# Optimization experiments

Hardware: AMD Instinct MI355X
Metric: run time of the kernel (lower is better)

Reference implementation:

```python
import jax, jax.numpy as jnp
import numpy as np

D_MODEL = 1024
N_HEADS = 16
HEAD_DIM = D_MODEL // N_HEADS
N_MEM = 16
EPS = 1e-5
ROPE_THETA = 10000.0


def layernorm(x, g, b):
    mu = jnp.mean(x, axis=-1, keepdims=True)
    var = jnp.mean(jnp.square(x - mu), axis=-1, keepdims=True)
    return (x - mu) * jax.lax.rsqrt(var + EPS) * g + b


def rope_cos_sin(seq_len, head_dim, dtype):
    inv_freq = 1.0 / (ROPE_THETA ** (jnp.arange(0, head_dim, 2, dtype=jnp.float32) / head_dim))
    pos = jnp.arange(seq_len, dtype=jnp.float32)
    freqs = pos[:, None] * inv_freq[None, :]            # [S, hd/2]
    emb = jnp.concatenate([freqs, freqs], axis=-1)       # [S, hd]
    return jnp.cos(emb).astype(dtype), jnp.sin(emb).astype(dtype)


def rotate_half(x):
    x1, x2 = jnp.split(x, 2, axis=-1)
    return jnp.concatenate([-x2, x1], axis=-1)


def setup_inputs() -> dict:
    key = jax.random.key(0)
    ks = jax.random.split(key, 8)
    B, T, D = 2, 2048, D_MODEL
    x = jax.random.normal(ks[0], (B, T, D), dtype=jnp.float32)
    memory_tokens = jax.random.normal(ks[1], (1, N_MEM, D), dtype=jnp.float32) * 0.02
    s = 1.0 / np.sqrt(D)
    qkv_w = jax.random.uniform(ks[2], (3 * D, D), minval=-s, maxval=s, dtype=jnp.float32)
    qkv_b = jax.random.uniform(ks[3], (3 * D,), minval=-s, maxval=s, dtype=jnp.float32)
    out_w = jax.random.uniform(ks[4], (D, D), minval=-s, maxval=s, dtype=jnp.float32)
    out_b = jax.random.uniform(ks[5], (D,), minval=-s, maxval=s, dtype=jnp.float32)
    norm_g = jnp.ones((D,), jnp.float32)
    norm_b = jnp.zeros((D,), jnp.float32)
    normm_g = jnp.ones((D,), jnp.float32)
    normm_b = jnp.zeros((D,), jnp.float32)
    return {"x": x, "memory_tokens": memory_tokens, "qkv_w": qkv_w, "qkv_b": qkv_b,
            "out_w": out_w, "out_b": out_b, "norm_g": norm_g, "norm_b": norm_b,
            "normm_g": normm_g, "normm_b": normm_b}


def reference(x, memory_tokens, qkv_w, qkv_b, out_w, out_b, norm_g, norm_b, normm_g, normm_b):
    B, T, D = x.shape
    S = N_MEM + T
    residual = x
    x_norm = layernorm(x, norm_g, norm_b)
    mem = layernorm(jnp.broadcast_to(memory_tokens, (B, N_MEM, D)), normm_g, normm_b)
    xm = jnp.concatenate([mem, x_norm], axis=1)                # [B, S, D]
    qkv = xm @ qkv_w.T + qkv_b                                 # [B, S, 3D]
    qkv = qkv.reshape(B, S, 3, N_HEADS, HEAD_DIM)
    q = jnp.transpose(qkv[:, :, 0], (0, 2, 1, 3))              # [B, H, S, hd]
    k = jnp.transpose(qkv[:, :, 1], (0, 2, 1, 3))
    v = jnp.transpose(qkv[:, :, 2], (0, 2, 1, 3))
    cos, sin = rope_cos_sin(S, HEAD_DIM, x.dtype)              # [S, hd]
    q = q * cos + rotate_half(q) * sin
    k = k * cos + rotate_half(k) * sin
    scale = 1.0 / np.sqrt(HEAD_DIM)
    scores = jnp.einsum("bhqd,bhkd->bhqk", q, k) * scale       # [B, H, S, S]
    causal = jnp.tril(jnp.ones((S, S), dtype=bool))
    scores = jnp.where(causal, scores, jnp.finfo(scores.dtype).min)
    attn = jax.nn.softmax(scores, axis=-1)
    out = jnp.einsum("bhqk,bhkd->bhqd", attn, v)               # [B, H, S, hd]
    out = jnp.transpose(out, (0, 2, 1, 3)).reshape(B, S, D)
    out = out @ out_w.T + out_b
    out = out[:, N_MEM:, :]
    return residual + out
```

## Files before the change

### kernel.cpp

```cpp
#include <hip/hip_runtime.h>
#include <cstdint>


using bf16 = __bf16;
typedef __attribute__((ext_vector_type(8))) __bf16 bf16x8;
typedef __attribute__((ext_vector_type(4))) __bf16 bf16x4;
typedef __attribute__((ext_vector_type(4))) float floatx4;

#define MFMA16(a, b, c) __builtin_amdgcn_mfma_f32_16x16x32_bf16(a, b, c, 0, 0, 0)

constexpr int SV = 2064;
constexpr int SP = 2112;
constexpr float LOG2_THETA = 13.287712379549449f;

__device__ __forceinline__ bool dt_is_bf16(const void* p) {
  return *(const uint32_t*)p == 0x3F803F80u;
}

struct f8 { float v[8]; };

__device__ __forceinline__ f8 load8(const void* p, size_t idx, bool bf) {
  f8 r;
  if (bf) {
    bf16x8 t = *(const bf16x8*)((const bf16*)p + idx);
#pragma unroll
    for (int j = 0; j < 8; ++j) r.v[j] = (float)t[j];
  } else {
    float4 a = *(const float4*)((const float*)p + idx);
    float4 b = *(const float4*)((const float*)p + idx + 4);
    r.v[0] = a.x; r.v[1] = a.y; r.v[2] = a.z; r.v[3] = a.w;
    r.v[4] = b.x; r.v[5] = b.y; r.v[6] = b.z; r.v[7] = b.w;
  }
  return r;
}

__device__ __forceinline__ float ld1(const void* p, size_t idx, bool bf) {
  return bf ? (float)((const bf16*)p)[idx] : ((const float*)p)[idx];
}

__device__ __forceinline__ void load16_to_lds(const bf16* gptr, bf16* lptr) {
  auto* g = reinterpret_cast<const __attribute__((address_space(1))) uint32_t*>(
      reinterpret_cast<uintptr_t>(gptr));
  auto* l = reinterpret_cast<__attribute__((address_space(3))) uint32_t*>(
      reinterpret_cast<uintptr_t>(lptr));
  __builtin_amdgcn_global_load_lds(g, l, 16, 0, 0);
}

__device__ __forceinline__ unsigned cvtpk_bf16(float lo, float hi) {
  unsigned r;
  asm("v_cvt_pk_bf16_f32 %0, %1, %2" : "=v"(r) : "v"(lo), "v"(hi));
  return r;
}

__global__ __launch_bounds__(256) void conv_w(
    const void* __restrict__ W, const void* __restrict__ flagp,
    bf16* __restrict__ dst) {
  const bool bf = dt_is_bf16(flagp);
  const size_t i = ((size_t)blockIdx.x * 256 + threadIdx.x) * 8;
  const f8 v = load8(W, i, bf);
  bf16x8 o;
#pragma unroll
  for (int j = 0; j < 8; ++j) o[j] = (bf16)v.v[j];
  *(bf16x8*)&dst[i] = o;
}

__global__ __launch_bounds__(256) void rope_tab(float2* __restrict__ tab) {
  const int i = blockIdx.x * 256 + threadIdx.x;
  const int pos = i >> 5, f = i & 31;
  const float ang = (float)pos * exp2f((float)f * (-LOG2_THETA / 32.0f));
  float c, s;
  sincosf(ang, &c, &s);
  tab[i] = make_float2(c, s);
}

__global__ __launch_bounds__(256) void ln_all(
    const void* __restrict__ x, const void* __restrict__ mem,
    const void* __restrict__ ng, const void* __restrict__ nb,
    const void* __restrict__ mg, const void* __restrict__ mb,
    bf16* __restrict__ mem16, bf16* __restrict__ xln) {
  const bool bf = dt_is_bf16(ng);
  const int t = threadIdx.x, wid = t >> 6, lane = t & 63;
  const int row = blockIdx.x * 4 + wid;
  const void *src, *g, *bb;
  size_t soff;
  bf16* out;
  if (row < 16) {
    src = mem; soff = (size_t)row * 1024; g = mg; bb = mb;
    out = mem16 + (size_t)row * 1024;
  } else {
    src = x; soff = (size_t)(row - 16) * 1024; g = ng; bb = nb;
    out = xln + (size_t)(row - 16) * 1024;
  }
  const f8 v0 = load8(src, soff + lane * 8, bf);
  const f8 v1 = load8(src, soff + 512 + lane * 8, bf);
  float sum = 0.f, sq = 0.f;
#pragma unroll
  for (int j = 0; j < 8; ++j) { sum += v0.v[j]; sq += v0.v[j] * v0.v[j]; }
#pragma unroll
  for (int j = 0; j < 8; ++j) { sum += v1.v[j]; sq += v1.v[j] * v1.v[j]; }
#pragma unroll
  for (int off = 1; off < 64; off <<= 1) {
    sum += __shfl_xor(sum, off);
    sq += __shfl_xor(sq, off);
  }
  const float mu = sum * (1.0f / 1024.0f);
  const float var = sq * (1.0f / 1024.0f) - mu * mu;
  const float rstd = rsqrtf(var + 1e-5f);
  const f8 g0 = load8(g, lane * 8, bf), g1 = load8(g, 512 + lane * 8, bf);
  const f8 b0 = load8(bb, lane * 8, bf), b1 = load8(bb, 512 + lane * 8, bf);
  bf16x8 o0, o1;
#pragma unroll
  for (int j = 0; j < 8; ++j) {
    o0[j] = (bf16)((v0.v[j] - mu) * rstd * g0.v[j] + b0.v[j]);
    o1[j] = (bf16)((v1.v[j] - mu) * rstd * g1.v[j] + b1.v[j]);
  }
  *(bf16x8*)&out[lane * 8] = o0;
  *(bf16x8*)&out[512 + lane * 8] = o1;
}

__global__ __launch_bounds__(512, 1) void gemm0_rope(
    const bf16* __restrict__ mem16, const bf16* __restrict__ xln,
    const bf16* __restrict__ Wqb, const void* __restrict__ bias,
    const void* __restrict__ flagp, const float2* __restrict__ rtab,
    bf16* __restrict__ Qg, bf16* __restrict__ Kg, bf16* __restrict__ Vg) {
  const bool bf = dt_is_bf16(flagp);
  __shared__ bf16 SH[65536];
  const int t = threadIdx.x;
  const int row0 = blockIdx.x * 256;
  const int col0 = blockIdx.y * 256;
  const int wid = t >> 6, lane = t & 63, lr = lane & 15, lg = lane >> 4;
  const int wm = wid >> 2, wn = wid & 3;
  const int xorv = (lr & 7) << 3;

  const int coff = (((t & 7) ^ ((t >> 3) & 7)) << 3);
  const bf16* aptr[4];
  const bf16* bptr[4];
#pragma unroll
  for (int s = 0; s < 4; ++s) {
    int g = row0 + s * 64 + (t >> 3);
    if (g > 4127) g = 4127;
    const int b2 = (g >= SV) ? 1 : 0;
    const int ss = g - b2 * SV;
    const bf16* ap = (ss < 16) ? (mem16 + (size_t)ss * 1024)
                               : (xln + ((size_t)(b2 * 2048 + ss - 16)) * 1024);
    aptr[s] = ap + coff;
    bptr[s] = Wqb + (size_t)(col0 + s * 64 + (t >> 3)) * 1024 + coff;
  }

  const int ldsbase = (t & ~63) * 8;
  auto STAGE = [&](int bufi, int k0) {
    bf16* Ld = SH + bufi * 32768;
#pragma unroll
    for (int s = 0; s < 4; ++s)
      load16_to_lds(aptr[s] + k0, Ld + s * 4096 + ldsbase);
#pragma unroll
    for (int s = 0; s < 4; ++s)
      load16_to_lds(bptr[s] + k0, Ld + 16384 + s * 4096 + ldsbase);
  };

  floatx4 acc[8][4] = {};
  STAGE(0, 0);
  STAGE(1, 64);

  for (int kt = 0; kt < 16; ++kt) {
    const int cur = kt & 1;
    if (kt < 15)
      asm volatile("s_waitcnt vmcnt(8)" ::: "memory");
    else
      asm volatile("s_waitcnt vmcnt(0)" ::: "memory");
    __builtin_amdgcn_s_barrier();
    __builtin_amdgcn_sched_barrier(0);
    const bf16* Ab = SH + cur * 32768;
    const bf16* Bb = Ab + 16384;
    bf16x8 a0[8], b0[4], a1[8], b1[4];
#pragma unroll
    for (int mi = 0; mi < 8; ++mi)
      a0[mi] = *(const bf16x8*)&Ab[(wm * 128 + mi * 16 + lr) * 64 + ((lg * 8) ^ xorv)];
#pragma unroll
    for (int ni = 0; ni < 4; ++ni)
      b0[ni] = *(const bf16x8*)&Bb[(wn * 64 + ni * 16 + lr) * 64 + ((lg * 8) ^ xorv)];
    __builtin_amdgcn_s_setprio(1);
#pragma unroll
    for (int mi = 0; mi < 8; ++mi)
#pragma unroll
      for (int ni = 0; ni < 4; ++ni)
        acc[mi][ni] = MFMA16(a0[mi], b0[ni], acc[mi][ni]);
    __builtin_amdgcn_s_setprio(0);
#pragma unroll
    for (int mi = 0; mi < 8; ++mi)
      a1[mi] = *(const bf16x8*)&Ab[(wm * 128 + mi * 16 + lr) * 64 + ((32 + lg * 8) ^ xorv)];
#pragma unroll
    for (int ni = 0; ni < 4; ++ni)
      b1[ni] = *(const bf16x8*)&Bb[(wn * 64 + ni * 16 + lr) * 64 + ((32 + lg * 8) ^ xorv)];
    __builtin_amdgcn_sched_barrier(0);
    asm volatile("s_waitcnt lgkmcnt(0)" ::: "memory");
    __builtin_amdgcn_s_barrier();
    __builtin_amdgcn_sched_barrier(0);
    if (kt < 14) STAGE(cur, (kt + 2) * 64);
    __builtin_amdgcn_s_setprio(1);
#pragma unroll
    for (int mi = 0; mi < 8; ++mi)
#pragma unroll
      for (int ni = 0; ni < 4; ++ni)
        acc[mi][ni] = MFMA16(a1[mi], b1[ni], acc[mi][ni]);
    __builtin_amdgcn_s_setprio(0);
  }

  const int colbase = col0 + wn * 64;
  const int part = colbase >> 10;
  const int h = (colbase >> 6) & 15;
  const int row0w = row0 + wm * 128;

  if (part == 2) {
#pragma unroll
    for (int mi = 0; mi < 8; ++mi) {
      const int gq = row0w + mi * 16 + lg * 4;
      if (gq >= 2 * SV) continue;
      const int b2 = (gq >= SV) ? 1 : 0;
      const int pos = gq - b2 * SV;
      const size_t hb = (size_t)(b2 * 16 + h) * 64;
#pragma unroll
      for (int ni = 0; ni < 4; ++ni) {
        const int d = ni * 16 + lr;
        const float bc = ld1(bias, colbase + ni * 16 + lr, bf);
        bf16x4 vv;
#pragma unroll
        for (int r = 0; r < 4; ++r) vv[r] = (bf16)(acc[mi][ni][r] + bc);
        *(bf16x4*)&Vg[(hb + d) * SP + pos] = vv;
      }
    }
  } else {
    bf16* Dst = (part == 0) ? Qg : Kg;
    const float qs = (part == 0) ? 0.18033688011f : 1.0f;
    float bv[4];
#pragma unroll
    for (int a = 0; a < 4; ++a) bv[a] = ld1(bias, colbase + a * 16 + lr, bf);
#pragma unroll
    for (int mi = 0; mi < 8; ++mi) {
#pragma unroll
      for (int r = 0; r < 4; ++r) {
        const int g = row0w + mi * 16 + lg * 4 + r;
        if (g >= 2 * SV) continue;
        const int b2 = (g >= SV) ? 1 : 0;
        const int pos = g - b2 * SV;
        bf16* drow = Dst + ((size_t)(b2 * 16 + h) * SP + pos) * 64;
#pragma unroll
        for (int a = 0; a < 2; ++a) {
          const float2 cs = rtab[pos * 32 + a * 16 + lr];
          const float vlo = (acc[mi][a][r] + bv[a]) * qs;
          const float vhi = (acc[mi][a + 2][r] + bv[a + 2]) * qs;
          drow[a * 16 + lr] = (bf16)(vlo * cs.x - vhi * cs.y);
          drow[32 + a * 16 + lr] = (bf16)(vhi * cs.x + vlo * cs.y);
        }
      }
    }
  }
}

__device__ __forceinline__ void softmax_pack(const floatx4* c, int qrow, int k0,
                                             bool nm, int lg, float& lsum,
                                             unsigned (&paw)[2][4]) {
  float pr[4][4];
#pragma unroll
  for (int j2 = 0; j2 < 4; ++j2) {
#pragma unroll
    for (int rr = 0; rr < 4; ++rr) {
      float s = c[j2][rr];
      if (nm && (k0 + j2 * 16 + lg * 4 + rr > qrow)) s = -1e30f;
      float p;
      asm("v_exp_f32 %0, %1" : "=v"(p) : "v"(s));
      lsum += p;
      pr[j2][rr] = p;
    }
  }
#pragma unroll
  for (int cc = 0; cc < 2; ++cc) {
#pragma unroll
    for (int p_ = 0; p_ < 2; ++p_) {
      unsigned a = cvtpk_bf16(pr[2 * cc][2 * p_], pr[2 * cc][2 * p_ + 1]);
      unsigned b2 = cvtpk_bf16(pr[2 * cc + 1][2 * p_], pr[2 * cc + 1][2 * p_ + 1]);
      asm("v_permlane32_swap_b32 %0, %1" : "+v"(a), "+v"(b2));
      asm("v_permlane16_swap_b32 %0, %1" : "+v"(a), "+v"(b2));
      paw[cc][p_] = a;
      paw[cc][2 + p_] = b2;
    }
  }
}

__global__ __launch_bounds__(256) void flash3(
    const bf16* __restrict__ Qg, const bf16* __restrict__ Kg,
    const bf16* __restrict__ Vg, bf16* __restrict__ attn_out) {
  const int st = 16 - blockIdx.x;
  const int bh = blockIdx.y;
  const int b = bh >> 4, h = bh & 15;
  const bf16* Qb = Qg + (size_t)bh * SP * 64;
  const bf16* Kb = Kg + (size_t)bh * SP * 64;
  const bf16* Vb = Vg + (size_t)bh * 64 * SP;

  const int t = threadIdx.x;
  const int wid = t >> 6, lane = t & 63, lr = lane & 15, lg = lane >> 4;
  const int qw0 = st * 128 + wid * 32;
  const int q0 = qw0 + lr, q1 = q0 + 16;
  const int nkt = min(2 * st + 2, 33);

  __shared__ bf16 Ks[2][64 * 72];
  __shared__ bf16 Vt[2][64 * 64];

  bf16x8 qf0a{}, qf0b{}, qf1a{}, qf1b{};
  if (q0 < SV) {
    qf0a = *(const bf16x8*)&Qb[(size_t)q0 * 64 + lg * 8];
    qf0b = *(const bf16x8*)&Qb[(size_t)q0 * 64 + 32 + lg * 8];
  }
  if (q1 < SV) {
    qf1a = *(const bf16x8*)&Qb[(size_t)q1 * 64 + lg * 8];
    qf1b = *(const bf16x8*)&Qb[(size_t)q1 * 64 + 32 + lg * 8];
  }

  floatx4 o0[4] = {}, o1[4] = {};
  float ls0 = 0.f, ls1 = 0.f;

  const int kr = t >> 2;
  const int kc = (t & 3) * 16;
  const int vd = t >> 2;
  const int vg0 = t & 3;
  const int vswz = ((vd & 7) ^ ((vd >> 4) & 3)) << 3;

  bf16x8 kA, kB, vA, vB;
  kA = *(const bf16x8*)&Kb[(size_t)kr * 64 + kc];
  kB = *(const bf16x8*)&Kb[(size_t)kr * 64 + kc + 8];
  vA = *(const bf16x8*)&Vb[(size_t)vd * SP + vg0 * 8];
  vB = *(const bf16x8*)&Vb[(size_t)vd * SP + (vg0 + 4) * 8];

  *(bf16x8*)&Ks[0][kr * 72 + kc] = kA;
  *(bf16x8*)&Ks[0][kr * 72 + kc + 8] = kB;
  *(bf16x8*)&Vt[0][vd * 64 + ((vg0 << 3) ^ vswz)] = vA;
  *(bf16x8*)&Vt[0][vd * 64 + (((vg0 + 4) << 3) ^ vswz)] = vB;
  kA = *(const bf16x8*)&Kb[(size_t)(64 + kr) * 64 + kc];
  kB = *(const bf16x8*)&Kb[(size_t)(64 + kr) * 64 + kc + 8];
  vA = *(const bf16x8*)&Vb[(size_t)vd * SP + 64 + vg0 * 8];
  vB = *(const bf16x8*)&Vb[(size_t)vd * SP + 64 + (vg0 + 4) * 8];
  asm volatile("s_waitcnt lgkmcnt(0)" ::: "memory");
  __builtin_amdgcn_s_barrier();
  __builtin_amdgcn_sched_barrier(0);

  for (int kt = 0; kt < nkt; ++kt) {
    const int cur = kt & 1;
    const int k0 = kt * 64;
    if (kt + 1 < nkt) {
      const int nb2 = cur ^ 1;
      *(bf16x8*)&Ks[nb2][kr * 72 + kc] = kA;
      *(bf16x8*)&Ks[nb2][kr * 72 + kc + 8] = kB;
      *(bf16x8*)&Vt[nb2][vd * 64 + ((vg0 << 3) ^ vswz)] = vA;
      *(bf16x8*)&Vt[nb2][vd * 64 + (((vg0 + 4) << 3) ^ vswz)] = vB;
      if (kt + 2 < nkt) {
        const int kn = k0 + 128;
        kA = *(const bf16x8*)&Kb[(size_t)(kn + kr) * 64 + kc];
        kB = *(const bf16x8*)&Kb[(size_t)(kn + kr) * 64 + kc + 8];
        vA = *(const bf16x8*)&Vb[(size_t)vd * SP + kn + vg0 * 8];
        vB = *(const bf16x8*)&Vb[(size_t)vd * SP + kn + (vg0 + 4) * 8];
      }
    }

    if (k0 <= qw0 + 31) {
      floatx4 c0[4] = {}, c1[4] = {};
      __builtin_amdgcn_s_setprio(1);
#pragma unroll
      for (int j2 = 0; j2 < 4; ++j2) {
        const bf16x8 kfa = *(const bf16x8*)&Ks[cur][(j2 * 16 + lr) * 72 + lg * 8];
        const bf16x8 kfb = *(const bf16x8*)&Ks[cur][(j2 * 16 + lr) * 72 + 32 + lg * 8];
        c0[j2] = MFMA16(kfa, qf0a, c0[j2]);
        c0[j2] = MFMA16(kfb, qf0b, c0[j2]);
        c1[j2] = MFMA16(kfa, qf1a, c1[j2]);
        c1[j2] = MFMA16(kfb, qf1b, c1[j2]);
      }
      __builtin_amdgcn_s_setprio(0);

      unsigned paw0[2][4], paw1[2][4];
      softmax_pack(c0, q0, k0, (k0 + 63 > qw0), lg, ls0, paw0);
      softmax_pack(c1, q1, k0, (k0 + 63 > qw0 + 16), lg, ls1, paw1);

      __builtin_amdgcn_s_setprio(1);
#pragma unroll
      for (int cc = 0; cc < 2; ++cc) {
        union { unsigned w[4]; bf16x8 v; } pu0, pu1;
#pragma unroll
        for (int i = 0; i < 4; ++i) { pu0.w[i] = paw0[cc][i]; pu1.w[i] = paw1[cc][i]; }
#pragma unroll
        for (int dt = 0; dt < 4; ++dt) {
          const int key8 = (cc * 32 + lg * 8) ^ ((((lr & 7) ^ dt)) << 3);
          const bf16x8 vf = *(const bf16x8*)&Vt[cur][(dt * 16 + lr) * 64 + key8];
          o0[dt] = MFMA16(pu0.v, vf, o0[dt]);
          o1[dt] = MFMA16(pu1.v, vf, o1[dt]);
        }
      }
      __builtin_amdgcn_s_setprio(0);
    }
    asm volatile("s_waitcnt lgkmcnt(0)" ::: "memory");
    __builtin_amdgcn_s_barrier();
    __builtin_amdgcn_sched_barrier(0);
  }

  float l0 = ls0, l1 = ls1;
  l0 += __shfl_xor(l0, 16); l0 += __shfl_xor(l0, 32);
  l1 += __shfl_xor(l1, 16); l1 += __shfl_xor(l1, 32);
#pragma unroll
  for (int r = 0; r < 4; ++r) {
    const float lv0 = __shfl(l0, lg * 4 + r);
    const float lv1 = __shfl(l1, lg * 4 + r);
    const int s0 = qw0 + lg * 4 + r;
    const int s1 = s0 + 16;
    if (s0 >= 16 && s0 < SV) {
      const float inv = 1.0f / lv0;
      const size_t rowoff = ((size_t)(b * 2048 + s0 - 16)) * 1024 + h * 64;
#pragma unroll
      for (int dt = 0; dt < 4; ++dt)
        attn_out[rowoff + dt * 16 + lr] = (bf16)(o0[dt][r] * inv);
    }
    if (s1 >= 16 && s1 < SV) {
      const float inv = 1.0f / lv1;
      const size_t rowoff = ((size_t)(b * 2048 + s1 - 16)) * 1024 + h * 64;
#pragma unroll
      for (int dt = 0; dt < 4; ++dt)
        attn_out[rowoff + dt * 16 + lr] = (bf16)(o1[dt][r] * inv);
    }
  }
}

__global__ __launch_bounds__(512, 1) void gemm1_proj(
    const bf16* __restrict__ A, const bf16* __restrict__ Wob,
    const void* __restrict__ bias, const void* __restrict__ x,
    const void* __restrict__ flagp, void* __restrict__ outp) {
  const bool bf = dt_is_bf16(flagp);
  __shared__ bf16 SH[32768];
  const int t = threadIdx.x;
  const int row0 = blockIdx.x * 128;
  const int col0 = blockIdx.y * 128;
  const int wid = t >> 6, lane = t & 63, lr = lane & 15, lg = lane >> 4;
  const int wm = wid >> 2, wn = wid & 3;
  const int xorv = (lr & 7) << 3;

  const int coff = (((t & 7) ^ ((t >> 3) & 7)) << 3);
  const bf16* aptr[2];
  const bf16* bptr[2];
#pragma unroll
  for (int s = 0; s < 2; ++s) {
    aptr[s] = A + (size_t)(row0 + s * 64 + (t >> 3)) * 1024 + coff;
    bptr[s] = Wob + (size_t)(col0 + s * 64 + (t >> 3)) * 1024 + coff;
  }
  const int ldsbase = (t & ~63) * 8;
  auto STAGE = [&](int bufi, int k0) {
    bf16* Ld = SH + bufi * 16384;
#pragma unroll
    for (int s = 0; s < 2; ++s)
      load16_to_lds(aptr[s] + k0, Ld + s * 4096 + ldsbase);
#pragma unroll
    for (int s = 0; s < 2; ++s)
      load16_to_lds(bptr[s] + k0, Ld + 8192 + s * 4096 + ldsbase);
  };

  floatx4 acc[4][2] = {};
  STAGE(0, 0);
  STAGE(1, 64);

  for (int kt = 0; kt < 16; ++kt) {
    const int cur = kt & 1;
    if (kt < 15)
      asm volatile("s_waitcnt vmcnt(4)" ::: "memory");
    else
      asm volatile("s_waitcnt vmcnt(0)" ::: "memory");
    __builtin_amdgcn_s_barrier();
    __builtin_amdgcn_sched_barrier(0);
    const bf16* Ab = SH + cur * 16384;
    const bf16* Bb = Ab + 8192;
    bf16x8 a0[4], b0[2], a1[4], b1[2];
#pragma unroll
    for (int mi = 0; mi < 4; ++mi)
      a0[mi] = *(const bf16x8*)&Ab[(wm * 64 + mi * 16 + lr) * 64 + ((lg * 8) ^ xorv)];
#pragma unroll
    for (int ni = 0; ni < 2; ++ni)
      b0[ni] = *(const bf16x8*)&Bb[(wn * 32 + ni * 16 + lr) * 64 + ((lg * 8) ^ xorv)];
    __builtin_amdgcn_s_setprio(1);
#pragma unroll
    for (int mi = 0; mi < 4; ++mi)
#pragma unroll
      for (int ni = 0; ni < 2; ++ni)
        acc[mi][ni] = MFMA16(a0[mi], b0[ni], acc[mi][ni]);
    __builtin_amdgcn_s_setprio(0);
#pragma unroll
    for (int mi = 0; mi < 4; ++mi)
      a1[mi] = *(const bf16x8*)&Ab[(wm * 64 + mi * 16 + lr) * 64 + ((32 + lg * 8) ^ xorv)];
#pragma unroll
    for (int ni = 0; ni < 2; ++ni)
      b1[ni] = *(const bf16x8*)&Bb[(wn * 32 + ni * 16 + lr) * 64 + ((32 + lg * 8) ^ xorv)];
    __builtin_amdgcn_sched_barrier(0);
    asm volatile("s_waitcnt lgkmcnt(0)" ::: "memory");
    __builtin_amdgcn_s_barrier();
    __builtin_amdgcn_sched_barrier(0);
    if (kt < 14) STAGE(cur, (kt + 2) * 64);
    __builtin_amdgcn_s_setprio(1);
#pragma unroll
    for (int mi = 0; mi < 4; ++mi)
#pragma unroll
      for (int ni = 0; ni < 2; ++ni)
        acc[mi][ni] = MFMA16(a1[mi], b1[ni], acc[mi][ni]);
    __builtin_amdgcn_s_setprio(0);
  }

#pragma unroll
  for (int mi = 0; mi < 4; ++mi) {
#pragma unroll
    for (int r = 0; r < 4; ++r) {
      const int row = row0 + wm * 64 + mi * 16 + lg * 4 + r;
#pragma unroll
      for (int ni = 0; ni < 2; ++ni) {
        const int col = col0 + wn * 32 + ni * 16 + lr;
        const size_t idx = (size_t)row * 1024 + col;
        const float v = acc[mi][ni][r] + ld1(bias, col, bf) + ld1(x, idx, bf);
        if (bf)
          ((bf16*)outp)[idx] = (bf16)v;
        else
          ((float*)outp)[idx] = v;
      }
    }
  }
}

extern "C" void kernel_launch(void* const* d_in, const int* in_sizes, int n_in,
                              void* d_out, int out_size, void* d_ws, size_t ws_size,
                              hipStream_t stream) {
  const void* x = d_in[0];
  const void* mem = d_in[1];
  const void* qkvw = d_in[2];
  const void* qkvb = d_in[3];
  const void* outw = d_in[4];
  const void* outb = d_in[5];
  const void* ng = d_in[6];
  const void* nb = d_in[7];
  const void* mg = d_in[8];
  const void* mb = d_in[9];

  char* ws = (char*)d_ws;
  bf16* mem16 = (bf16*)(ws);
  bf16* xln = (bf16*)(ws + 32768);
  bf16* Qg = (bf16*)(ws + 8421376);
  bf16* Kg = (bf16*)(ws + 17072128);
  bf16* Vg = (bf16*)(ws + 25722880);
  bf16* Wqb = (bf16*)(ws + 34373632);
  bf16* Wob = (bf16*)(ws + 40665088);
  bf16* attn = xln;
  float2* rtab = (float2*)Wob;

  conv_w<<<1536, 256, 0, stream>>>(qkvw, ng, Wqb);
  ln_all<<<1028, 256, 0, stream>>>(x, mem, ng, nb, mg, mb, mem16, xln);
  rope_tab<<<258, 256, 0, stream>>>(rtab);
  gemm0_rope<<<dim3(17, 12), 512, 0, stream>>>(mem16, xln, Wqb, qkvb, ng, rtab,
                                               Qg, Kg, Vg);
  conv_w<<<512, 256, 0, stream>>>(outw, ng, Wob);
  flash3<<<dim3(17, 32), 256, 0, stream>>>(Qg, Kg, Vg, attn);
  gemm1_proj<<<dim3(32, 8), 512, 0, stream>>>(attn, Wob, outb, x, ng, d_out);
}
```

Measured before the change: 228.6 us.

## Rewrite attention as LDS-free per-wave kernel with XCD-aware block mapping

Replaces the shared-memory double-buffered flash kernel (128-query tiles, two 16-row groups per wave) with one that uses 64-query tiles and a single 16-row group per wave. Each wave loads K and V fragments straight from global memory into registers, with no LDS staging and no barriers. Blocks are remapped to a linear grid so that heads are grouped per XCD for L2 locality, and the longest query tiles are scheduled first. A new zero_pad kernel clears the padded rows of Q, K and V, since the loads now read past the valid sequence without guards. The trade-off is fewer barriers and more parallelism, against redundant global/L2 traffic for K and V across the four waves of a block.

```diff
diff --git a/kernel.cpp b/kernel.cpp
--- a/kernel.cpp
+++ b/kernel.cpp
@@ -71,6 +71,23 @@
   float c, s;
   sincosf(ang, &c, &s);
   tab[i] = make_float2(c, s);
+}
+
+__global__ __launch_bounds__(256) void zero_pad(
+    bf16* __restrict__ Qg, bf16* __restrict__ Kg, bf16* __restrict__ Vg) {
+  const int bh = blockIdx.x / 3;
+  const int arr = blockIdx.x % 3;
+  const int t = threadIdx.x;
+  const bf16x8 z{};
+  if (arr < 2) {
+    bf16* base = (arr == 0 ? Qg : Kg) + ((size_t)bh * SP + SV) * 64;
+    for (int j = t; j < 384; j += 256) *(bf16x8*)&base[j * 8] = z;
+  } else {
+    for (int j = t; j < 384; j += 256) {
+      const int d = j / 6, c = (j % 6) * 8;
+      *(bf16x8*)&Vg[((size_t)bh * 64 + d) * SP + SV + c] = z;
+    }
+  }
 }
 
 __global__ __launch_bounds__(256) void ln_all(
@@ -257,41 +274,14 @@
   }
 }
 
-__device__ __forceinline__ void softmax_pack(const floatx4* c, int qrow, int k0,
-                                             bool nm, int lg, float& lsum,
-                                             unsigned (&paw)[2][4]) {
-  float pr[4][4];
-#pragma unroll
-  for (int j2 = 0; j2 < 4; ++j2) {
-#pragma unroll
-    for (int rr = 0; rr < 4; ++rr) {
-      float s = c[j2][rr];
-      if (nm && (k0 + j2 * 16 + lg * 4 + rr > qrow)) s = -1e30f;
-      float p;
-      asm("v_exp_f32 %0, %1" : "=v"(p) : "v"(s));
-      lsum += p;
-      pr[j2][rr] = p;
-    }
-  }
-#pragma unroll
-  for (int cc = 0; cc < 2; ++cc) {
-#pragma unroll
-    for (int p_ = 0; p_ < 2; ++p_) {
-      unsigned a = cvtpk_bf16(pr[2 * cc][2 * p_], pr[2 * cc][2 * p_ + 1]);
-      unsigned b2 = cvtpk_bf16(pr[2 * cc + 1][2 * p_], pr[2 * cc + 1][2 * p_ + 1]);
-      asm("v_permlane32_swap_b32 %0, %1" : "+v"(a), "+v"(b2));
-      asm("v_permlane16_swap_b32 %0, %1" : "+v"(a), "+v"(b2));
-      paw[cc][p_] = a;
-      paw[cc][2 + p_] = b2;
-    }
-  }
-}
-
-__global__ __launch_bounds__(256) void flash3(
+__global__ __launch_bounds__(256) void flash4(
     const bf16* __restrict__ Qg, const bf16* __restrict__ Kg,
     const bf16* __restrict__ Vg, bf16* __restrict__ attn_out) {
-  const int st = 16 - blockIdx.x;
-  const int bh = blockIdx.y;
+  const int lin = blockIdx.x;
+  const int xcd = lin & 7;
+  const int idx = lin >> 3;
+  const int qt = 32 - (idx >> 2);
+  const int bh = ((idx & 3) << 3) | xcd;
   const int b = bh >> 4, h = bh & 15;
   const bf16* Qb = Qg + (size_t)bh * SP * 64;
   const bf16* Kb = Kg + (size_t)bh * SP * 64;
@@ -299,130 +289,99 @@
 
   const int t = threadIdx.x;
   const int wid = t >> 6, lane = t & 63, lr = lane & 15, lg = lane >> 4;
-  const int qw0 = st * 128 + wid * 32;
-  const int q0 = qw0 + lr, q1 = q0 + 16;
-  const int nkt = min(2 * st + 2, 33);
-
-  __shared__ bf16 Ks[2][64 * 72];
-  __shared__ bf16 Vt[2][64 * 64];
-
-  bf16x8 qf0a{}, qf0b{}, qf1a{}, qf1b{};
-  if (q0 < SV) {
-    qf0a = *(const bf16x8*)&Qb[(size_t)q0 * 64 + lg * 8];
-    qf0b = *(const bf16x8*)&Qb[(size_t)q0 * 64 + 32 + lg * 8];
-  }
-  if (q1 < SV) {
-    qf1a = *(const bf16x8*)&Qb[(size_t)q1 * 64 + lg * 8];
-    qf1b = *(const bf16x8*)&Qb[(size_t)q1 * 64 + 32 + lg * 8];
-  }
-
-  floatx4 o0[4] = {}, o1[4] = {};
-  float ls0 = 0.f, ls1 = 0.f;
-
-  const int kr = t >> 2;
-  const int kc = (t & 3) * 16;
-  const int vd = t >> 2;
-  const int vg0 = t & 3;
-  const int vswz = ((vd & 7) ^ ((vd >> 4) & 3)) << 3;
-
-  bf16x8 kA, kB, vA, vB;
-  kA = *(const bf16x8*)&Kb[(size_t)kr * 64 + kc];
-  kB = *(const bf16x8*)&Kb[(size_t)kr * 64 + kc + 8];
-  vA = *(const bf16x8*)&Vb[(size_t)vd * SP + vg0 * 8];
-  vB = *(const bf16x8*)&Vb[(size_t)vd * SP + (vg0 + 4) * 8];
-
-  *(bf16x8*)&Ks[0][kr * 72 + kc] = kA;
-  *(bf16x8*)&Ks[0][kr * 72 + kc + 8] = kB;
-  *(bf16x8*)&Vt[0][vd * 64 + ((vg0 << 3) ^ vswz)] = vA;
-  *(bf16x8*)&Vt[0][vd * 64 + (((vg0 + 4) << 3) ^ vswz)] = vB;
-  kA = *(const bf16x8*)&Kb[(size_t)(64 + kr) * 64 + kc];
-  kB = *(const bf16x8*)&Kb[(size_t)(64 + kr) * 64 + kc + 8];
-  vA = *(const bf16x8*)&Vb[(size_t)vd * SP + 64 + vg0 * 8];
-  vB = *(const bf16x8*)&Vb[(size_t)vd * SP + 64 + (vg0 + 4) * 8];
-  asm volatile("s_waitcnt lgkmcnt(0)" ::: "memory");
-  __builtin_amdgcn_s_barrier();
-  __builtin_amdgcn_sched_barrier(0);
-
-  for (int kt = 0; kt < nkt; ++kt) {
-    const int cur = kt & 1;
+  const int qw0 = qt * 64 + wid * 16;
+  const int q = qw0 + lr;
+
+  bf16x8 qf0{}, qf1{};
+  if (q < SV) {
+    qf0 = *(const bf16x8*)&Qb[(size_t)q * 64 + lg * 8];
+    qf1 = *(const bf16x8*)&Qb[(size_t)q * 64 + 32 + lg * 8];
+  }
+
+  floatx4 o[4] = {};
+  float lsum = 0.f;
+
+  const bf16* kbase = Kb + lr * 64 + lg * 8;
+  const bf16* vbase = Vb + (size_t)lr * SP + lg * 8;
+
+  for (int kt = 0; kt <= qt; ++kt) {
     const int k0 = kt * 64;
-    if (kt + 1 < nkt) {
-      const int nb2 = cur ^ 1;
-      *(bf16x8*)&Ks[nb2][kr * 72 + kc] = kA;
-      *(bf16x8*)&Ks[nb2][kr * 72 + kc + 8] = kB;
-      *(bf16x8*)&Vt[nb2][vd * 64 + ((vg0 << 3) ^ vswz)] = vA;
-      *(bf16x8*)&Vt[nb2][vd * 64 + (((vg0 + 4) << 3) ^ vswz)] = vB;
-      if (kt + 2 < nkt) {
-        const int kn = k0 + 128;
-        kA = *(const bf16x8*)&Kb[(size_t)(kn + kr) * 64 + kc];
-        kB = *(const bf16x8*)&Kb[(size_t)(kn + kr) * 64 + kc + 8];
-        vA = *(const bf16x8*)&Vb[(size_t)vd * SP + kn + vg0 * 8];
-        vB = *(const bf16x8*)&Vb[(size_t)vd * SP + kn + (vg0 + 4) * 8];
+
+    const bf16* kp = kbase + k0 * 64;
+    bf16x8 kfa[4], kfb[4];
+#pragma unroll
+    for (int j2 = 0; j2 < 4; ++j2) {
+      kfa[j2] = *(const bf16x8*)&kp[j2 * 1024];
+      kfb[j2] = *(const bf16x8*)&kp[j2 * 1024 + 32];
+    }
+    floatx4 c[4] = {};
+#pragma unroll
+    for (int j2 = 0; j2 < 4; ++j2) {
+      c[j2] = MFMA16(kfa[j2], qf0, c[j2]);
+      c[j2] = MFMA16(kfb[j2], qf1, c[j2]);
+    }
+
+    bf16x8 vf[2][4];
+#pragma unroll
+    for (int dt = 0; dt < 4; ++dt) {
+      const bf16* vp = vbase + (size_t)dt * 16 * SP + k0;
+      vf[0][dt] = *(const bf16x8*)&vp[0];
+      vf[1][dt] = *(const bf16x8*)&vp[32];
+    }
+
+    const bool nm = (k0 + 63 > qw0);
+    float pr[4][4];
+#pragma unroll
+    for (int j2 = 0; j2 < 4; ++j2) {
+#pragma unroll
+      for (int rr = 0; rr < 4; ++rr) {
+        float s = c[j2][rr];
+        if (nm && (k0 + j2 * 16 + lg * 4 + rr > q)) s = -1e30f;
+        float p;
+        asm("v_exp_f32 %0, %1" : "=v"(p) : "v"(s));
+        lsum += p;
+        pr[j2][rr] = p;
       }
     }
 
-    if (k0 <= qw0 + 31) {
-      floatx4 c0[4] = {}, c1[4] = {};
-      __builtin_amdgcn_s_setprio(1);
-#pragma unroll
-      for (int j2 = 0; j2 < 4; ++j2) {
-        const bf16x8 kfa = *(const bf16x8*)&Ks[cur][(j2 * 16 + lr) * 72 + lg * 8];
-        const bf16x8 kfb = *(const bf16x8*)&Ks[cur][(j2 * 16 + lr) * 72 + 32 + lg * 8];
-        c0[j2] = MFMA16(kfa, qf0a, c0[j2]);
-        c0[j2] = MFMA16(kfb, qf0b, c0[j2]);
-        c1[j2] = MFMA16(kfa, qf1a, c1[j2]);
-        c1[j2] = MFMA16(kfb, qf1b, c1[j2]);
+    unsigned paw[2][4];
+#pragma unroll
+    for (int cc = 0; cc < 2; ++cc) {
+#pragma unroll
+      for (int p_ = 0; p_ < 2; ++p_) {
+        unsigned a = cvtpk_bf16(pr[2 * cc][2 * p_], pr[2 * cc][2 * p_ + 1]);
+        unsigned b2 = cvtpk_bf16(pr[2 * cc + 1][2 * p_], pr[2 * cc + 1][2 * p_ + 1]);
+        asm("v_permlane32_swap_b32 %0, %1" : "+v"(a), "+v"(b2));
+        asm("v_permlane16_swap_b32 %0, %1" : "+v"(a), "+v"(b2));
+        paw[cc][p_] = a;
+        paw[cc][2 + p_] = b2;
       }
-      __builtin_amdgcn_s_setprio(0);
-
-      unsigned paw0[2][4], paw1[2][4];
-      softmax_pack(c0, q0, k0, (k0 + 63 > qw0), lg, ls0, paw0);
-      softmax_pack(c1, q1, k0, (k0 + 63 > qw0 + 16), lg, ls1, paw1);
-
-      __builtin_amdgcn_s_setprio(1);
-#pragma unroll
-      for (int cc = 0; cc < 2; ++cc) {
-        union { unsigned w[4]; bf16x8 v; } pu0, pu1;
-#pragma unroll
-        for (int i = 0; i < 4; ++i) { pu0.w[i] = paw0[cc][i]; pu1.w[i] = paw1[cc][i]; }
-#pragma unroll
-        for (int dt = 0; dt < 4; ++dt) {
-          const int key8 = (cc * 32 + lg * 8) ^ ((((lr & 7) ^ dt)) << 3);
-          const bf16x8 vf = *(const bf16x8*)&Vt[cur][(dt * 16 + lr) * 64 + key8];
-          o0[dt] = MFMA16(pu0.v, vf, o0[dt]);
-          o1[dt] = MFMA16(pu1.v, vf, o1[dt]);
-        }
-      }
-      __builtin_amdgcn_s_setprio(0);
-    }
-    asm volatile("s_waitcnt lgkmcnt(0)" ::: "memory");
-    __builtin_amdgcn_s_barrier();
-    __builtin_amdgcn_sched_barrier(0);
-  }
-
-  float l0 = ls0, l1 = ls1;
-  l0 += __shfl_xor(l0, 16); l0 += __shfl_xor(l0, 32);
-  l1 += __shfl_xor(l1, 16); l1 += __shfl_xor(l1, 32);
+    }
+
+#pragma unroll
+    for (int cc = 0; cc < 2; ++cc) {
+      union { unsigned w[4]; bf16x8 v; } pu;
+      pu.w[0] = paw[cc][0]; pu.w[1] = paw[cc][1];
+      pu.w[2] = paw[cc][2]; pu.w[3] = paw[cc][3];
+#pragma unroll
+      for (int dt = 0; dt < 4; ++dt)
+        o[dt] = MFMA16(pu.v, vf[cc][dt], o[dt]);
+    }
+  }
+
+  float l = lsum;
+  l += __shfl_xor(l, 16);
+  l += __shfl_xor(l, 32);
 #pragma unroll
   for (int r = 0; r < 4; ++r) {
-    const float lv0 = __shfl(l0, lg * 4 + r);
-    const float lv1 = __shfl(l1, lg * 4 + r);
-    const int s0 = qw0 + lg * 4 + r;
-    const int s1 = s0 + 16;
-    if (s0 >= 16 && s0 < SV) {
-      const float inv = 1.0f / lv0;
-      const size_t rowoff = ((size_t)(b * 2048 + s0 - 16)) * 1024 + h * 64;
-#pragma unroll
-      for (int dt = 0; dt < 4; ++dt)
-        attn_out[rowoff + dt * 16 + lr] = (bf16)(o0[dt][r] * inv);
-    }
-    if (s1 >= 16 && s1 < SV) {
-      const float inv = 1.0f / lv1;
-      const size_t rowoff = ((size_t)(b * 2048 + s1 - 16)) * 1024 + h * 64;
-#pragma unroll
-      for (int dt = 0; dt < 4; ++dt)
-        attn_out[rowoff + dt * 16 + lr] = (bf16)(o1[dt][r] * inv);
-    }
+    const float lv = __shfl(l, lg * 4 + r);
+    const int s = qw0 + lg * 4 + r;
+    if (s < 16 || s >= SV) continue;
+    const float inv = 1.0f / lv;
+    const size_t rowoff = ((size_t)(b * 2048 + s - 16)) * 1024 + h * 64;
+#pragma unroll
+    for (int dt = 0; dt < 4; ++dt)
+      attn_out[rowoff + dt * 16 + lr] = (bf16)(o[dt][r] * inv);
   }
 }
 
@@ -553,9 +512,10 @@
   conv_w<<<1536, 256, 0, stream>>>(qkvw, ng, Wqb);
   ln_all<<<1028, 256, 0, stream>>>(x, mem, ng, nb, mg, mb, mem16, xln);
   rope_tab<<<258, 256, 0, stream>>>(rtab);
+  zero_pad<<<96, 256, 0, stream>>>(Qg, Kg, Vg);
   gemm0_rope<<<dim3(17, 12), 512, 0, stream>>>(mem16, xln, Wqb, qkvb, ng, rtab,
                                                Qg, Kg, Vg);
   conv_w<<<512, 256, 0, stream>>>(outw, ng, Wob);
-  flash3<<<dim3(17, 32), 256, 0, stream>>>(Qg, Kg, Vg, attn);
+  flash4<<<1056, 256, 0, stream>>>(Qg, Kg, Vg, attn);
   gemm1_proj<<<dim3(32, 8), 512, 0, stream>>>(attn, Wob, outb, x, ng, d_out);
 }
```

Measured after the change: 312.2 us. 1.37x slower.
